# Optimization experiments

Hardware: AMD Instinct MI355X
Metric: run time of the kernel (lower is better)

Reference implementation:

```python
import jax, jax.numpy as jnp
import numpy as np

K, D, BETA = 64, 512, 100.0
EPS = 1e-12  # F.normalize default eps


def setup_inputs() -> dict:
    key = jax.random.key(0)
    kx, kc = jax.random.split(key)
    x = jax.random.normal(kx, (32, D, 32, 32), dtype=jnp.float32)
    centroids = jax.random.uniform(kc, (K, D), dtype=jnp.float32)  # torch.rand init
    conv_w = 2.0 * BETA * centroids                                # conv weight [K, D] (1x1 kernel)
    conv_b = -BETA * jnp.linalg.norm(centroids, axis=1)            # conv bias [K]
    return {"x": x, "centroids": centroids, "conv_w": conv_w, "conv_b": conv_b}


def reference(x, centroids, conv_w, conv_b):
    N, C = x.shape[:2]
    xf = x.reshape(N, C, -1)                                  # [N, D, P], P = H*W
    # 1x1 conv == per-pixel linear: logits [N, K, P]
    logits = jnp.einsum('ndp,kd->nkp', xf, conv_w) + conv_b[None, :, None]
    a = jax.nn.softmax(logits, axis=1)                        # soft assignment over clusters
    # residual-sum collapses algebraically:
    # vlad[n,k,d] = sum_p a[n,k,p]*x[n,d,p] - (sum_p a[n,k,p]) * c[k,d]
    vlad = jnp.einsum('nkp,ndp->nkd', a, xf) - a.sum(-1)[:, :, None] * centroids[None]
    # intra-normalize per cluster (dim=2), then flatten and L2-normalize
    vlad = vlad / jnp.maximum(jnp.linalg.norm(vlad, axis=2, keepdims=True), EPS)
    vlad = vlad.reshape(N, -1)
    vlad = vlad / jnp.maximum(jnp.linalg.norm(vlad, axis=1, keepdims=True), EPS)
    return vlad
```

## Files before the change

### kernel.cpp

```cpp
#include <hip/hip_runtime.h>
#include <math.h>


namespace {

constexpr int NI   = 32;
constexpr int DIMC = 512;
constexpr int KCL  = 64;
constexpr int PIXN = 1024;
constexpr float EPSF = 1e-12f;

#define AS1 __attribute__((address_space(1)))
#define AS3 __attribute__((address_space(3)))

__device__ __forceinline__ void glds16(const float* g, float* l) {
  __builtin_amdgcn_global_load_lds((const AS1 void*)g, (AS3 void*)l, 16, 0, 0);
}

__global__ __launch_bounds__(256) void k0_wt(const float* __restrict__ w,
                                             float* __restrict__ wt) {
  const int i = blockIdx.x * 256 + threadIdx.x;
  wt[i] = w[(size_t)(i & 63) * DIMC + (i >> 6)];
}

__global__ __launch_bounds__(256, 2) void k1a_logits(
    const float* __restrict__ x, const float* __restrict__ wt,
    const float* __restrict__ conv_b, float* __restrict__ A)
{
  __shared__ float smem[16384];
  float* const xs0 = smem;
  float* const wl0 = smem + 8192;
  float* const scr = smem;

  const int tid = threadIdx.x;
  const int w  = __builtin_amdgcn_readfirstlane(tid >> 6);
  const int l  = tid & 63;
  const int lk = l & 7, ld = l >> 3;
  const int bid = blockIdx.x;
  const int xcd = bid & 7, rest = bid >> 3;
  const int n  = xcd + ((rest & 3) << 3);
  const int pg = rest >> 2;
  const int pb = pg << 6;

  const float* xn = x + (size_t)n * DIMC * PIXN + pb;

#pragma unroll
  for (int s = 0; s < 4; ++s) {
    const int i = s * 256 + tid;
    glds16(xn + (size_t)(i >> 4) * PIXN + ((i & 15) << 2), xs0 + (i << 2));
    glds16(wt + (i << 2), wl0 + (i << 2));
  }

  float acc[8][8];
#pragma unroll
  for (int i = 0; i < 8; ++i)
#pragma unroll
    for (int j = 0; j < 8; ++j) acc[i][j] = 0.0f;

  for (int ch = 0; ch < 8; ++ch) {
    const int cur = ch & 1;
    __syncthreads();
    if (ch < 7) {
      const float* xc = xn + (size_t)((ch + 1) * 64) * PIXN;
      const float* wc = wt + (ch + 1) * 4096;
#pragma unroll
      for (int s = 0; s < 4; ++s) {
        const int i = s * 256 + tid;
        glds16(xc + (size_t)(i >> 4) * PIXN + ((i & 15) << 2),
               xs0 + (cur ^ 1) * 4096 + (i << 2));
        glds16(wc + (i << 2), wl0 + (cur ^ 1) * 4096 + (i << 2));
      }
    }
    const float* wr = wl0 + cur * 4096 + (w << 10) + (lk << 3);
    const float* xr = xs0 + cur * 4096 + (w << 10) + (ld << 3);
#pragma unroll 4
    for (int dd = 0; dd < 16; ++dd) {
      const float4 wa = *reinterpret_cast<const float4*>(wr + (dd << 6));
      const float4 wb = *reinterpret_cast<const float4*>(wr + (dd << 6) + 4);
      const float4 xa = *reinterpret_cast<const float4*>(xr + (dd << 6));
      const float4 xb = *reinterpret_cast<const float4*>(xr + (dd << 6) + 4);
      const float wv[8] = {wa.x, wa.y, wa.z, wa.w, wb.x, wb.y, wb.z, wb.w};
      const float xv[8] = {xa.x, xa.y, xa.z, xa.w, xb.x, xb.y, xb.z, xb.w};
#pragma unroll
      for (int i = 0; i < 8; ++i)
#pragma unroll
        for (int j = 0; j < 8; ++j)
          acc[i][j] = fmaf(wv[i], xv[j], acc[i][j]);
    }
  }
  __syncthreads();

#define TST(RB)                                                              \
  do {                                                                       \
    _Pragma("unroll") for (int i = 0; i < 8; ++i) {                          \
      *reinterpret_cast<float4*>((RB) + ((2 * i) << 8) + (l << 2)) =         \
          make_float4(acc[i][0], acc[i][1], acc[i][2], acc[i][3]);           \
      *reinterpret_cast<float4*>((RB) + ((2 * i + 1) << 8) + (l << 2)) =     \
          make_float4(acc[i][4], acc[i][5], acc[i][6], acc[i][7]);           \
    }                                                                        \
  } while (0)
#define TADD(RB)                                                             \
  do {                                                                       \
    _Pragma("unroll") for (int i = 0; i < 8; ++i) {                          \
      const float4 t0 = *reinterpret_cast<const float4*>(                    \
          (RB) + ((2 * i) << 8) + (l << 2));                                 \
      const float4 t1 = *reinterpret_cast<const float4*>(                    \
          (RB) + ((2 * i + 1) << 8) + (l << 2));                             \
      acc[i][0] += t0.x; acc[i][1] += t0.y; acc[i][2] += t0.z;               \
      acc[i][3] += t0.w; acc[i][4] += t1.x; acc[i][5] += t1.y;               \
      acc[i][6] += t1.z; acc[i][7] += t1.w;                                  \
    }                                                                        \
  } while (0)

  if (w == 1) TST(scr);
  if (w == 3) TST(scr + 4096);
  __syncthreads();
  if (w == 0) TADD(scr);
  if (w == 2) TADD(scr + 4096);
  __syncthreads();
  if (w == 2) TST(scr);
  __syncthreads();

  if (w == 0) {
    TADD(scr);
    const float4 b0 = *reinterpret_cast<const float4*>(conv_b + (lk << 3));
    const float4 b1 = *reinterpret_cast<const float4*>(conv_b + (lk << 3) + 4);
    const float bv[8] = {b0.x, b0.y, b0.z, b0.w, b1.x, b1.y, b1.z, b1.w};
#pragma unroll
    for (int i = 0; i < 8; ++i)
#pragma unroll
      for (int j = 0; j < 8; ++j) acc[i][j] += bv[i];
    float m[8], S[8];
#pragma unroll
    for (int j = 0; j < 8; ++j) {
      m[j] = acc[0][j];
#pragma unroll
      for (int i = 1; i < 8; ++i) m[j] = fmaxf(m[j], acc[i][j]);
      m[j] = fmaxf(m[j], __shfl_xor(m[j], 1, 64));
      m[j] = fmaxf(m[j], __shfl_xor(m[j], 2, 64));
      m[j] = fmaxf(m[j], __shfl_xor(m[j], 4, 64));
      S[j] = 0.0f;
#pragma unroll
      for (int i = 0; i < 8; ++i) {
        acc[i][j] = __expf(acc[i][j] - m[j]);
        S[j] += acc[i][j];
      }
      S[j] += __shfl_xor(S[j], 1, 64);
      S[j] += __shfl_xor(S[j], 2, 64);
      S[j] += __shfl_xor(S[j], 4, 64);
      S[j] = 1.0f / S[j];
    }
    const int bq = ((ld << 1) ^ lk) & ~1;
#pragma unroll
    for (int i = 0; i < 8; ++i) {
      const float4 lo = make_float4(acc[i][0] * S[0], acc[i][1] * S[1],
                                    acc[i][2] * S[2], acc[i][3] * S[3]);
      const float4 hi = make_float4(acc[i][4] * S[4], acc[i][5] * S[5],
                                    acc[i][6] * S[6], acc[i][7] * S[7]);
      float* arow = A + ((size_t)n * KCL + (lk << 3) + i) * PIXN + pb + (bq << 2);
      if (lk & 1) {
        *reinterpret_cast<float4*>(arow)     = hi;
        *reinterpret_cast<float4*>(arow + 4) = lo;
      } else {
        *reinterpret_cast<float4*>(arow)     = lo;
        *reinterpret_cast<float4*>(arow + 4) = hi;
      }
    }
  }
#undef TST
#undef TADD
}

__global__ __launch_bounds__(512, 2) void k2a_vlad(
    const float* __restrict__ x, const float* __restrict__ A,
    const float* __restrict__ cent, float* __restrict__ out,
    float* __restrict__ ssqp)
{
  __shared__ float smem[18432];
  float* const aL0 = smem;
  float* const xL0 = smem + 8192;
  float* const scr = smem;

  const int tid = threadIdx.x;
  const int w  = __builtin_amdgcn_readfirstlane(tid >> 6);
  const int l  = tid & 63;
  const int lk = l & 7, ld = l >> 3;
  const int bid = blockIdx.x;
  const int xcd = bid & 7, rest = bid >> 3;
  const int n  = xcd + ((rest & 3) << 3);
  const int dt = rest >> 2;
  const int d0 = dt << 6;

  const float* an = A + (size_t)n * (KCL * PIXN);
  const float* xn = x + ((size_t)n * DIMC + d0) * PIXN;
  const int i0 = tid, i1 = tid + 512;
  const int xq0 = ((i0 & 15) ^ (i0 >> 7)) << 2;
  const int xq1 = (((i1 & 15) ^ (i1 >> 7)) & 15) << 2;

  glds16(an + (size_t)(i0 >> 4) * PIXN + ((i0 & 15) << 2), aL0 + (i0 << 2));
  glds16(an + (size_t)(i1 >> 4) * PIXN + ((i1 & 15) << 2), aL0 + (i1 << 2));
  glds16(xn + (size_t)(i0 >> 4) * PIXN + xq0, xL0 + (i0 << 2));
  glds16(xn + (size_t)(i1 >> 4) * PIXN + xq1, xL0 + (i1 << 2));

  float acc[8][8], sacc[8];
#pragma unroll
  for (int i = 0; i < 8; ++i) {
    sacc[i] = 0.0f;
#pragma unroll
    for (int j = 0; j < 8; ++j) acc[i][j] = 0.0f;
  }
  __syncthreads();

  for (int ch = 0; ch < 16; ++ch) {
    const int cur = ch & 1;
    const float* aLc = aL0 + cur * 4096;
    const float* xLc = xL0 + cur * 4096;
    if (ch < 15) {
      const int c2 = (ch + 1) * 64;
      float* aLn = aL0 + (cur ^ 1) * 4096;
      float* xLn = xL0 + (cur ^ 1) * 4096;
      glds16(an + (size_t)(i0 >> 4) * PIXN + c2 + ((i0 & 15) << 2), aLn + (i0 << 2));
      glds16(an + (size_t)(i1 >> 4) * PIXN + c2 + ((i1 & 15) << 2), aLn + (i1 << 2));
      glds16(xn + (size_t)(i0 >> 4) * PIXN + c2 + xq0, xLn + (i0 << 2));
      glds16(xn + (size_t)(i1 >> 4) * PIXN + c2 + xq1, xLn + (i1 << 2));
    }
#pragma unroll
    for (int q = 0; q < 2; ++q) {
      const int pq = (w << 1) + q;
      float4 af[8], xf[8];
#pragma unroll
      for (int i = 0; i < 8; ++i)
        af[i] = *reinterpret_cast<const float4*>(
            aLc + (((lk << 3) + i) << 6) + ((pq ^ lk) << 2));
#pragma unroll
      for (int jd = 0; jd < 8; ++jd)
        xf[jd] = *reinterpret_cast<const float4*>(
            xLc + (((ld << 3) + jd) << 6) + ((pq ^ ld) << 2));
#pragma unroll
      for (int i = 0; i < 8; ++i) {
        sacc[i] += ((af[i].x + af[i].y) + af[i].z) + af[i].w;
#pragma unroll
        for (int jd = 0; jd < 8; ++jd) {
          acc[i][jd] = fmaf(af[i].x, xf[jd].x, acc[i][jd]);
          acc[i][jd] = fmaf(af[i].y, xf[jd].y, acc[i][jd]);
          acc[i][jd] = fmaf(af[i].z, xf[jd].z, acc[i][jd]);
          acc[i][jd] = fmaf(af[i].w, xf[jd].w, acc[i][jd]);
        }
      }
    }
    __syncthreads();
  }

#define TST(RB)                                                              \
  do {                                                                       \
    _Pragma("unroll") for (int i = 0; i < 8; ++i) {                          \
      *reinterpret_cast<float4*>((RB) + ((2 * i) << 8) + (l << 2)) =         \
          make_float4(acc[i][0], acc[i][1], acc[i][2], acc[i][3]);           \
      *reinterpret_cast<float4*>((RB) + ((2 * i + 1) << 8) + (l << 2)) =     \
          make_float4(acc[i][4], acc[i][5], acc[i][6], acc[i][7]);           \
    }                                                                        \
    *reinterpret_cast<float4*>((RB) + (16 << 8) + (l << 2)) =                \
        make_float4(sacc[0], sacc[1], sacc[2], sacc[3]);                     \
    *reinterpret_cast<float4*>((RB) + (17 << 8) + (l << 2)) =                \
        make_float4(sacc[4], sacc[5], sacc[6], sacc[7]);                     \
  } while (0)
#define TADD(RB)                                                             \
  do {                                                                       \
    _Pragma("unroll") for (int i = 0; i < 8; ++i) {                          \
      const float4 t0 = *reinterpret_cast<const float4*>(                    \
          (RB) + ((2 * i) << 8) + (l << 2));                                 \
      const float4 t1 = *reinterpret_cast<const float4*>(                    \
          (RB) + ((2 * i + 1) << 8) + (l << 2));                             \
      acc[i][0] += t0.x; acc[i][1] += t0.y; acc[i][2] += t0.z;               \
      acc[i][3] += t0.w; acc[i][4] += t1.x; acc[i][5] += t1.y;               \
      acc[i][6] += t1.z; acc[i][7] += t1.w;                                  \
    }                                                                        \
    const float4 s0 = *reinterpret_cast<const float4*>(                      \
        (RB) + (16 << 8) + (l << 2));                                        \
    const float4 s1 = *reinterpret_cast<const float4*>(                      \
        (RB) + (17 << 8) + (l << 2));                                        \
    sacc[0] += s0.x; sacc[1] += s0.y; sacc[2] += s0.z; sacc[3] += s0.w;      \
    sacc[4] += s1.x; sacc[5] += s1.y; sacc[6] += s1.z; sacc[7] += s1.w;      \
  } while (0)

  if (w >= 4) TST(scr + (w - 4) * 4608);
  __syncthreads();
  if (w < 4) TADD(scr + w * 4608);
  __syncthreads();
  if (w == 2) TST(scr);
  if (w == 3) TST(scr + 4608);
  __syncthreads();
  if (w < 2) TADD(scr + w * 4608);
  __syncthreads();
  if (w == 1) TST(scr);
  __syncthreads();

  if (w == 0) {
    TADD(scr);
#pragma unroll
    for (int i = 0; i < 8; ++i) {
      const int k = (lk << 3) + i;
      const float s = sacc[i];
      const float* cp = cent + (size_t)k * DIMC + d0 + (ld << 3);
      const float4 c0 = *reinterpret_cast<const float4*>(cp);
      const float4 c1 = *reinterpret_cast<const float4*>(cp + 4);
      float r[8];
      r[0] = acc[i][0] - s * c0.x; r[1] = acc[i][1] - s * c0.y;
      r[2] = acc[i][2] - s * c0.z; r[3] = acc[i][3] - s * c0.w;
      r[4] = acc[i][4] - s * c1.x; r[5] = acc[i][5] - s * c1.y;
      r[6] = acc[i][6] - s * c1.z; r[7] = acc[i][7] - s * c1.w;
      float* op = out + ((size_t)n * KCL + k) * DIMC + d0 + (ld << 3);
      *reinterpret_cast<float4*>(op)     = make_float4(r[0], r[1], r[2], r[3]);
      *reinterpret_cast<float4*>(op + 4) = make_float4(r[4], r[5], r[6], r[7]);
      float q = 0.0f;
#pragma unroll
      for (int j = 0; j < 8; ++j) q = fmaf(r[j], r[j], q);
      q += __shfl_xor(q, 8, 64);
      q += __shfl_xor(q, 16, 64);
      q += __shfl_xor(q, 32, 64);
      if (ld == 0) ssqp[((size_t)n * KCL + k) * 8 + dt] = q;
    }
  }
#undef TST
#undef TADD
}

__global__ __launch_bounds__(256) void k2c_norm(
    const float* __restrict__ ssqp, float* __restrict__ out)
{
  __shared__ float invs[64];
  __shared__ float gsh;
  const int tid = threadIdx.x;
  const int n  = blockIdx.x >> 3;
  const int kc = blockIdx.x & 7;
  if (tid < 64) {
    float ssq = 0.0f;
#pragma unroll
    for (int dt = 0; dt < 8; ++dt)
      ssq += ssqp[((size_t)n * KCL + tid) * 8 + dt];
    const float inv = 1.0f / fmaxf(sqrtf(ssq), EPSF);
    invs[tid] = inv;
    float rqv = ssq * inv * inv;
#pragma unroll
    for (int off = 32; off > 0; off >>= 1) rqv += __shfl_xor(rqv, off, 64);
    if (tid == 0) gsh = 1.0f / fmaxf(sqrtf(rqv), EPSF);
  }
  __syncthreads();
  const float sc = invs[(kc << 3) + (tid >> 5)] * gsh;
  float* o = out + ((size_t)n * KCL + (kc << 3)) * DIMC + tid * 16;
#pragma unroll
  for (int q = 0; q < 4; ++q) {
    float4 v = *reinterpret_cast<float4*>(o + (q << 2));
    v.x *= sc; v.y *= sc; v.z *= sc; v.w *= sc;
    *reinterpret_cast<float4*>(o + (q << 2)) = v;
  }
}

}

extern "C" void kernel_launch(void* const* d_in, const int* in_sizes, int n_in,
                              void* d_out, int out_size, void* d_ws, size_t ws_size,
                              hipStream_t stream) {
  (void)in_sizes; (void)n_in; (void)out_size; (void)ws_size;
  const float* x      = (const float*)d_in[0];
  const float* cent   = (const float*)d_in[1];
  const float* conv_w = (const float*)d_in[2];
  const float* conv_b = (const float*)d_in[3];
  float* out = (float*)d_out;
  float* ws  = (float*)d_ws;

  float* A    = ws;
  float* wt   = A + (size_t)NI * PIXN * KCL;
  float* ssqp = wt + 32768;

  k0_wt     <<<128, 256, 0, stream>>>(conv_w, wt);
  k1a_logits<<<512, 256, 0, stream>>>(x, wt, conv_b, A);
  k2a_vlad  <<<256, 512, 0, stream>>>(x, A, cent, out, ssqp);
  k2c_norm  <<<256, 256, 0, stream>>>(ssqp, out);
}
```

Before: 92.31 us.

## Double threads per block in logits and VLAD GEMM kernels with deeper wave reductions

Both GEMM-style kernels now launch twice as many waves per block: k1a_logits goes to 512 threads and k2a_vlad to 1024. Each wave handles a smaller slice of the reduction dimension per tile, and the cross-wave partial-sum reduction through LDS gains extra stages. The aim is more latency hiding and fewer per-thread global-to-LDS copies. In exchange, the stricter launch bounds (4 blocks per CU at 512 and 1024 threads) put heavy pressure on registers, which risks spilling the 64-float accumulator tile. The longer reduction tree also adds barriers and LDS traffic.

```diff
diff --git a/kernel.cpp b/kernel.cpp
--- a/kernel.cpp
+++ b/kernel.cpp
@@ -23,7 +23,7 @@
   wt[i] = w[(size_t)(i & 63) * DIMC + (i >> 6)];
 }
 
-__global__ __launch_bounds__(256, 2) void k1a_logits(
+__global__ __launch_bounds__(512, 4) void k1a_logits(
     const float* __restrict__ x, const float* __restrict__ wt,
     const float* __restrict__ conv_b, float* __restrict__ A)
 {
@@ -43,13 +43,12 @@
   const int pb = pg << 6;
 
   const float* xn = x + (size_t)n * DIMC * PIXN + pb;
-
-#pragma unroll
-  for (int s = 0; s < 4; ++s) {
-    const int i = s * 256 + tid;
-    glds16(xn + (size_t)(i >> 4) * PIXN + ((i & 15) << 2), xs0 + (i << 2));
-    glds16(wt + (i << 2), wl0 + (i << 2));
-  }
+  const int i0 = tid, i1 = tid + 512;
+
+  glds16(xn + (size_t)(i0 >> 4) * PIXN + ((i0 & 15) << 2), xs0 + (i0 << 2));
+  glds16(xn + (size_t)(i1 >> 4) * PIXN + ((i1 & 15) << 2), xs0 + (i1 << 2));
+  glds16(wt + (i0 << 2), wl0 + (i0 << 2));
+  glds16(wt + (i1 << 2), wl0 + (i1 << 2));
 
   float acc[8][8];
 #pragma unroll
@@ -63,18 +62,17 @@
     if (ch < 7) {
       const float* xc = xn + (size_t)((ch + 1) * 64) * PIXN;
       const float* wc = wt + (ch + 1) * 4096;
-#pragma unroll
-      for (int s = 0; s < 4; ++s) {
-        const int i = s * 256 + tid;
-        glds16(xc + (size_t)(i >> 4) * PIXN + ((i & 15) << 2),
-               xs0 + (cur ^ 1) * 4096 + (i << 2));
-        glds16(wc + (i << 2), wl0 + (cur ^ 1) * 4096 + (i << 2));
-      }
-    }
-    const float* wr = wl0 + cur * 4096 + (w << 10) + (lk << 3);
-    const float* xr = xs0 + cur * 4096 + (w << 10) + (ld << 3);
-#pragma unroll 4
-    for (int dd = 0; dd < 16; ++dd) {
+      glds16(xc + (size_t)(i0 >> 4) * PIXN + ((i0 & 15) << 2),
+             xs0 + (cur ^ 1) * 4096 + (i0 << 2));
+      glds16(xc + (size_t)(i1 >> 4) * PIXN + ((i1 & 15) << 2),
+             xs0 + (cur ^ 1) * 4096 + (i1 << 2));
+      glds16(wc + (i0 << 2), wl0 + (cur ^ 1) * 4096 + (i0 << 2));
+      glds16(wc + (i1 << 2), wl0 + (cur ^ 1) * 4096 + (i1 << 2));
+    }
+    const float* wr = wl0 + cur * 4096 + (w << 9) + (lk << 3);
+    const float* xr = xs0 + cur * 4096 + (w << 9) + (ld << 3);
+#pragma unroll
+    for (int dd = 0; dd < 8; ++dd) {
       const float4 wa = *reinterpret_cast<const float4*>(wr + (dd << 6));
       const float4 wb = *reinterpret_cast<const float4*>(wr + (dd << 6) + 4);
       const float4 xa = *reinterpret_cast<const float4*>(xr + (dd << 6));
@@ -112,13 +110,19 @@
     }                                                                        \
   } while (0)
 
+  if (w == 4) TST(scr);
+  if (w == 5) TST(scr + 4096);
+  if (w == 6) TST(scr + 8192);
+  if (w == 7) TST(scr + 12288);
+  __syncthreads();
+  if (w < 4) TADD(scr + w * 4096);
+  __syncthreads();
+  if (w == 2) TST(scr);
+  if (w == 3) TST(scr + 4096);
+  __syncthreads();
+  if (w < 2) TADD(scr + w * 4096);
+  __syncthreads();
   if (w == 1) TST(scr);
-  if (w == 3) TST(scr + 4096);
-  __syncthreads();
-  if (w == 0) TADD(scr);
-  if (w == 2) TADD(scr + 4096);
-  __syncthreads();
-  if (w == 2) TST(scr);
   __syncthreads();
 
   if (w == 0) {
@@ -171,7 +175,7 @@
 #undef TADD
 }
 
-__global__ __launch_bounds__(512, 2) void k2a_vlad(
+__global__ __launch_bounds__(1024, 4) void k2a_vlad(
     const float* __restrict__ x, const float* __restrict__ A,
     const float* __restrict__ cent, float* __restrict__ out,
     float* __restrict__ ssqp)
@@ -193,21 +197,19 @@
 
   const float* an = A + (size_t)n * (KCL * PIXN);
   const float* xn = x + ((size_t)n * DIMC + d0) * PIXN;
-  const int i0 = tid, i1 = tid + 512;
-  const int xq0 = ((i0 & 15) ^ (i0 >> 7)) << 2;
-  const int xq1 = (((i1 & 15) ^ (i1 >> 7)) & 15) << 2;
-
-  glds16(an + (size_t)(i0 >> 4) * PIXN + ((i0 & 15) << 2), aL0 + (i0 << 2));
-  glds16(an + (size_t)(i1 >> 4) * PIXN + ((i1 & 15) << 2), aL0 + (i1 << 2));
-  glds16(xn + (size_t)(i0 >> 4) * PIXN + xq0, xL0 + (i0 << 2));
-  glds16(xn + (size_t)(i1 >> 4) * PIXN + xq1, xL0 + (i1 << 2));
+  const int i = tid;
+  const int arow = i >> 4, aq = (i & 15) << 2;
+  const int xq = (((i & 15) ^ (i >> 7)) & 15) << 2;
+
+  glds16(an + (size_t)arow * PIXN + aq, aL0 + (i << 2));
+  glds16(xn + (size_t)arow * PIXN + xq, xL0 + (i << 2));
 
   float acc[8][8], sacc[8];
 #pragma unroll
-  for (int i = 0; i < 8; ++i) {
-    sacc[i] = 0.0f;
-#pragma unroll
-    for (int j = 0; j < 8; ++j) acc[i][j] = 0.0f;
+  for (int ii = 0; ii < 8; ++ii) {
+    sacc[ii] = 0.0f;
+#pragma unroll
+    for (int j = 0; j < 8; ++j) acc[ii][j] = 0.0f;
   }
   __syncthreads();
 
@@ -217,35 +219,27 @@
     const float* xLc = xL0 + cur * 4096;
     if (ch < 15) {
       const int c2 = (ch + 1) * 64;
-      float* aLn = aL0 + (cur ^ 1) * 4096;
-      float* xLn = xL0 + (cur ^ 1) * 4096;
-      glds16(an + (size_t)(i0 >> 4) * PIXN + c2 + ((i0 & 15) << 2), aLn + (i0 << 2));
-      glds16(an + (size_t)(i1 >> 4) * PIXN + c2 + ((i1 & 15) << 2), aLn + (i1 << 2));
-      glds16(xn + (size_t)(i0 >> 4) * PIXN + c2 + xq0, xLn + (i0 << 2));
-      glds16(xn + (size_t)(i1 >> 4) * PIXN + c2 + xq1, xLn + (i1 << 2));
-    }
-#pragma unroll
-    for (int q = 0; q < 2; ++q) {
-      const int pq = (w << 1) + q;
-      float4 af[8], xf[8];
-#pragma unroll
-      for (int i = 0; i < 8; ++i)
-        af[i] = *reinterpret_cast<const float4*>(
-            aLc + (((lk << 3) + i) << 6) + ((pq ^ lk) << 2));
-#pragma unroll
-      for (int jd = 0; jd < 8; ++jd)
-        xf[jd] = *reinterpret_cast<const float4*>(
-            xLc + (((ld << 3) + jd) << 6) + ((pq ^ ld) << 2));
-#pragma unroll
-      for (int i = 0; i < 8; ++i) {
-        sacc[i] += ((af[i].x + af[i].y) + af[i].z) + af[i].w;
-#pragma unroll
-        for (int jd = 0; jd < 8; ++jd) {
-          acc[i][jd] = fmaf(af[i].x, xf[jd].x, acc[i][jd]);
-          acc[i][jd] = fmaf(af[i].y, xf[jd].y, acc[i][jd]);
-          acc[i][jd] = fmaf(af[i].z, xf[jd].z, acc[i][jd]);
-          acc[i][jd] = fmaf(af[i].w, xf[jd].w, acc[i][jd]);
-        }
+      glds16(an + (size_t)arow * PIXN + c2 + aq,
+             aL0 + (cur ^ 1) * 4096 + (i << 2));
+      glds16(xn + (size_t)arow * PIXN + c2 + xq,
+             xL0 + (cur ^ 1) * 4096 + (i << 2));
+    }
+    float4 xf[8];
+#pragma unroll
+    for (int jd = 0; jd < 8; ++jd)
+      xf[jd] = *reinterpret_cast<const float4*>(
+          xLc + (((ld << 3) + jd) << 6) + ((w ^ ld) << 2));
+#pragma unroll
+    for (int ii = 0; ii < 8; ++ii) {
+      const float4 af = *reinterpret_cast<const float4*>(
+          aLc + (((lk << 3) + ii) << 6) + ((w ^ lk) << 2));
+      sacc[ii] += ((af.x + af.y) + af.z) + af.w;
+#pragma unroll
+      for (int jd = 0; jd < 8; ++jd) {
+        acc[ii][jd] = fmaf(af.x, xf[jd].x, acc[ii][jd]);
+        acc[ii][jd] = fmaf(af.y, xf[jd].y, acc[ii][jd]);
+        acc[ii][jd] = fmaf(af.z, xf[jd].z, acc[ii][jd]);
+        acc[ii][jd] = fmaf(af.w, xf[jd].w, acc[ii][jd]);
       }
     }
     __syncthreads();
@@ -253,11 +247,11 @@
 
 #define TST(RB)                                                              \
   do {                                                                       \
-    _Pragma("unroll") for (int i = 0; i < 8; ++i) {                          \
-      *reinterpret_cast<float4*>((RB) + ((2 * i) << 8) + (l << 2)) =         \
-          make_float4(acc[i][0], acc[i][1], acc[i][2], acc[i][3]);           \
-      *reinterpret_cast<float4*>((RB) + ((2 * i + 1) << 8) + (l << 2)) =     \
-          make_float4(acc[i][4], acc[i][5], acc[i][6], acc[i][7]);           \
+    _Pragma("unroll") for (int ii = 0; ii < 8; ++ii) {                       \
+      *reinterpret_cast<float4*>((RB) + ((2 * ii) << 8) + (l << 2)) =        \
+          make_float4(acc[ii][0], acc[ii][1], acc[ii][2], acc[ii][3]);       \
+      *reinterpret_cast<float4*>((RB) + ((2 * ii + 1) << 8) + (l << 2)) =    \
+          make_float4(acc[ii][4], acc[ii][5], acc[ii][6], acc[ii][7]);       \
     }                                                                        \
     *reinterpret_cast<float4*>((RB) + (16 << 8) + (l << 2)) =                \
         make_float4(sacc[0], sacc[1], sacc[2], sacc[3]);                     \
@@ -266,14 +260,14 @@
   } while (0)
 #define TADD(RB)                                                             \
   do {                                                                       \
-    _Pragma("unroll") for (int i = 0; i < 8; ++i) {                          \
+    _Pragma("unroll") for (int ii = 0; ii < 8; ++ii) {                       \
       const float4 t0 = *reinterpret_cast<const float4*>(                    \
-          (RB) + ((2 * i) << 8) + (l << 2));                                 \
+          (RB) + ((2 * ii) << 8) + (l << 2));                                \
       const float4 t1 = *reinterpret_cast<const float4*>(                    \
-          (RB) + ((2 * i + 1) << 8) + (l << 2));                             \
-      acc[i][0] += t0.x; acc[i][1] += t0.y; acc[i][2] += t0.z;               \
-      acc[i][3] += t0.w; acc[i][4] += t1.x; acc[i][5] += t1.y;               \
-      acc[i][6] += t1.z; acc[i][7] += t1.w;                                  \
+          (RB) + ((2 * ii + 1) << 8) + (l << 2));                            \
+      acc[ii][0] += t0.x; acc[ii][1] += t0.y; acc[ii][2] += t0.z;            \
+      acc[ii][3] += t0.w; acc[ii][4] += t1.x; acc[ii][5] += t1.y;            \
+      acc[ii][6] += t1.z; acc[ii][7] += t1.w;                                \
     }                                                                        \
     const float4 s0 = *reinterpret_cast<const float4*>(                      \
         (RB) + (16 << 8) + (l << 2));                                        \
@@ -283,7 +277,15 @@
     sacc[4] += s1.x; sacc[5] += s1.y; sacc[6] += s1.z; sacc[7] += s1.w;      \
   } while (0)
 
-  if (w >= 4) TST(scr + (w - 4) * 4608);
+  if (w >= 8 && w < 12) TST(scr + (w - 8) * 4608);
+  __syncthreads();
+  if (w < 4) TADD(scr + w * 4608);
+  __syncthreads();
+  if (w >= 12) TST(scr + (w - 12) * 4608);
+  __syncthreads();
+  if (w >= 4 && w < 8) TADD(scr + (w - 4) * 4608);
+  __syncthreads();
+  if (w >= 4 && w < 8) TST(scr + (w - 4) * 4608);
   __syncthreads();
   if (w < 4) TADD(scr + w * 4608);
   __syncthreads();
@@ -298,17 +300,17 @@
   if (w == 0) {
     TADD(scr);
 #pragma unroll
-    for (int i = 0; i < 8; ++i) {
-      const int k = (lk << 3) + i;
-      const float s = sacc[i];
+    for (int ii = 0; ii < 8; ++ii) {
+      const int k = (lk << 3) + ii;
+      const float s = sacc[ii];
       const float* cp = cent + (size_t)k * DIMC + d0 + (ld << 3);
       const float4 c0 = *reinterpret_cast<const float4*>(cp);
       const float4 c1 = *reinterpret_cast<const float4*>(cp + 4);
       float r[8];
-      r[0] = acc[i][0] - s * c0.x; r[1] = acc[i][1] - s * c0.y;
-      r[2] = acc[i][2] - s * c0.z; r[3] = acc[i][3] - s * c0.w;
-      r[4] = acc[i][4] - s * c1.x; r[5] = acc[i][5] - s * c1.y;
-      r[6] = acc[i][6] - s * c1.z; r[7] = acc[i][7] - s * c1.w;
+      r[0] = acc[ii][0] - s * c0.x; r[1] = acc[ii][1] - s * c0.y;
+      r[2] = acc[ii][2] - s * c0.z; r[3] = acc[ii][3] - s * c0.w;
+      r[4] = acc[ii][4] - s * c1.x; r[5] = acc[ii][5] - s * c1.y;
+      r[6] = acc[ii][6] - s * c1.z; r[7] = acc[ii][7] - s * c1.w;
       float* op = out + ((size_t)n * KCL + k) * DIMC + d0 + (ld << 3);
       *reinterpret_cast<float4*>(op)     = make_float4(r[0], r[1], r[2], r[3]);
       *reinterpret_cast<float4*>(op + 4) = make_float4(r[4], r[5], r[6], r[7]);
@@ -373,8 +375,8 @@
   float* wt   = A + (size_t)NI * PIXN * KCL;
   float* ssqp = wt + 32768;
 
-  k0_wt     <<<128, 256, 0, stream>>>(conv_w, wt);
-  k1a_logits<<<512, 256, 0, stream>>>(x, wt, conv_b, A);
-  k2a_vlad  <<<256, 512, 0, stream>>>(x, A, cent, out, ssqp);
-  k2c_norm  <<<256, 256, 0, stream>>>(ssqp, out);
-}
+  k0_wt     <<<128,  256, 0, stream>>>(conv_w, wt);
+  k1a_logits<<<512,  512, 0, stream>>>(x, wt, conv_b, A);
+  k2a_vlad  <<<256, 1024, 0, stream>>>(x, A, cent, out, ssqp);
+  k2c_norm  <<<256,  256, 0, stream>>>(ssqp, out);
+}
```

New measurement: 165.5 us. 1.79x slower.
